# Kernel optimization log

Hardware: AMD Instinct MI355X
Metric: run time of the kernel (lower is better)

## Reference

```python
import jax, jax.numpy as jnp
import numpy as np

DIM, NHEADS, HEAD_DIM = 1536, 12, 128
EPS = 1e-6
ROPE_SPLIT = (22, 21, 21)  # head_dim//2 = 64 -> (c-2*(c//3), c//3, c//3)


def setup_inputs() -> dict:
    key = jax.random.key(0)
    ks = jax.random.split(key, 12)
    B, F, H, W = 1, 8, 16, 28
    L = F * H * W  # 3584
    inp = {
        "x": jax.random.normal(ks[0], (B, L, DIM), jnp.float32),
        "seq_lens": jnp.full((B,), L, dtype=jnp.int64),
        "grid_sizes": jnp.array([[F, H, W]] * B, dtype=jnp.int64),
        "freqs": jax.random.uniform(ks[1], (1024, HEAD_DIM // 2), jnp.float32) * (2 * np.pi),
        "Wq": jax.random.normal(ks[2], (DIM, DIM), jnp.float32) / np.sqrt(DIM),
        "bq": jnp.zeros((DIM,), jnp.float32),
        "Wk": jax.random.normal(ks[3], (DIM, DIM), jnp.float32) / np.sqrt(DIM),
        "bk": jnp.zeros((DIM,), jnp.float32),
        "Wv": jax.random.normal(ks[4], (DIM, DIM), jnp.float32) / np.sqrt(DIM),
        "bv": jnp.zeros((DIM,), jnp.float32),
        "Wo": jax.random.normal(ks[5], (DIM, DIM), jnp.float32) / np.sqrt(DIM),
        "bo": jnp.zeros((DIM,), jnp.float32),
        "gq": jnp.ones((DIM,), jnp.float32),
        "gk": jnp.ones((DIM,), jnp.float32),
    }
    return inp


def _rms_norm(x, g):
    var = jnp.mean(jnp.square(x), axis=-1, keepdims=True)
    return x * jax.lax.rsqrt(var + EPS) * g


def _rope_angles(freqs, F, H, W):
    # freqs: [1024, 64] angles; split per 3D axis and broadcast over the grid
    cf, ch, cw = ROPE_SPLIT
    af = freqs[:F, :cf]
    ah = freqs[:H, cf:cf + ch]
    aw = freqs[:W, cf + ch:]
    ang = jnp.concatenate([
        jnp.broadcast_to(af[:, None, None, :], (F, H, W, cf)),
        jnp.broadcast_to(ah[None, :, None, :], (F, H, W, ch)),
        jnp.broadcast_to(aw[None, None, :, :], (F, H, W, cw)),
    ], axis=-1).reshape(F * H * W, cf + ch + cw)  # [L, 64]
    return jnp.cos(ang), jnp.sin(ang)


def _rope_apply(x, cos, sin):
    # x: [B, L, N, D]; complex multiply by unit-modulus freqs, in real arithmetic
    b, s, n, d = x.shape
    xr = x.reshape(b, s, n, d // 2, 2)
    a, bi = xr[..., 0], xr[..., 1]
    c = cos[None, :, None, :]
    si = sin[None, :, None, :]
    out = jnp.stack([a * c - bi * si, a * si + bi * c], axis=-1)
    return out.reshape(b, s, n, d)


def reference(x, seq_lens, grid_sizes, freqs, Wq, bq, Wk, bk, Wv, bv, Wo, bo, gq, gk):
    b, s, _ = x.shape
    n, d = NHEADS, HEAD_DIM
    gs = np.asarray(grid_sizes)
    F, H, W = int(gs[0, 0]), int(gs[0, 1]), int(gs[0, 2])  # static grid (same per batch)

    q = _rms_norm(x @ Wq + bq, gq).reshape(b, s, n, d)
    k = _rms_norm(x @ Wk + bk, gk).reshape(b, s, n, d)
    v = (x @ Wv + bv).reshape(b, s, n, d)

    cos, sin = _rope_angles(freqs, F, H, W)
    q = _rope_apply(q, cos, sin)
    k = _rope_apply(k, cos, sin)

    # full attention with key-length masking (flash_attention k_lens semantics)
    scale = 1.0 / np.sqrt(d)
    scores = jnp.einsum("bqnd,bknd->bnqk", q, k) * scale
    key_mask = jnp.arange(s)[None, :] < seq_lens[:, None]  # [B, S]
    scores = jnp.where(key_mask[:, None, None, :], scores, -1e9)
    probs = jax.nn.softmax(scores, axis=-1)
    out = jnp.einsum("bnqk,bknd->bqnd", probs, v)

    return out.reshape(b, s, n * d) @ Wo + bo
```

## Files before the change

kernel.cpp:

```cpp
#include <hip/hip_runtime.h>

typedef __bf16 bf16;
typedef __bf16 bf16x8 __attribute__((ext_vector_type(8)));
typedef __bf16 bf16x4 __attribute__((ext_vector_type(4)));
typedef float f32x4 __attribute__((ext_vector_type(4)));

__device__ __forceinline__ void gload_lds16(const void* g, void* l) {
  __builtin_amdgcn_global_load_lds(
      (const __attribute__((address_space(1))) void*)g,
      (__attribute__((address_space(3))) void*)l, 16, 0, 0);
}

__device__ __forceinline__ bf16x8 ld8(const bf16* p) {
  bf16x8 v; __builtin_memcpy(&v, p, 16); return v;
}

__global__ __launch_bounds__(256) void prologue(
    const float* __restrict__ x, const float* __restrict__ Wq, const float* __restrict__ Wk,
    const float* __restrict__ Wv, const float* __restrict__ Wo,
    const float* __restrict__ freqs, const int* __restrict__ gs,
    const float* __restrict__ bq, const float* __restrict__ bk, const float* __restrict__ bv,
    bf16* __restrict__ x_bf, bf16* __restrict__ wqkvt, bf16* __restrict__ wot,
    float* __restrict__ tabc, float* __restrict__ tabs, float* __restrict__ bqkv) {
  __shared__ bf16 tile[64][72];
  int b = blockIdx.x, t = threadIdx.x;
  if (b < 2688) {
    int i = b * 256 + t;
    const float4* p = (const float4*)x + (size_t)i * 2;
    float4 a = p[0], v2 = p[1];
    bf16x8 o;
    o[0] = (bf16)a.x;  o[1] = (bf16)a.y;  o[2] = (bf16)a.z;  o[3] = (bf16)a.w;
    o[4] = (bf16)v2.x; o[5] = (bf16)v2.y; o[6] = (bf16)v2.z; o[7] = (bf16)v2.w;
    *((bf16x8*)x_bf + i) = o;
  } else if (b < 4992) {
    const float* W; bf16* dstM; int xy;
    if (b < 4416) {
      int idx = b - 2688; int z = idx / 576; xy = idx % 576;
      W = (z == 0) ? Wq : (z == 1) ? Wk : Wv;
      dstM = wqkvt + (size_t)z * 1536 * 1536;
    } else {
      xy = b - 4416; W = Wo; dstM = wot;
    }
    int k0 = (xy % 24) * 64, n0 = (xy / 24) * 64;
    int r = t >> 2, c0 = (t & 3) * 16;
    const float* src = W + (size_t)(k0 + r) * 1536 + n0 + c0;
#pragma unroll
    for (int q = 0; q < 4; ++q) {
      float4 v = *(const float4*)(src + q * 4);
      tile[c0 + q * 4 + 0][r] = (bf16)v.x;
      tile[c0 + q * 4 + 1][r] = (bf16)v.y;
      tile[c0 + q * 4 + 2][r] = (bf16)v.z;
      tile[c0 + q * 4 + 3][r] = (bf16)v.w;
    }
    __syncthreads();
    bf16* dst = dstM + (size_t)(n0 + r) * 1536 + k0 + c0;
    bf16x8 o0, o1;
#pragma unroll
    for (int j = 0; j < 8; ++j) { o0[j] = tile[r][c0 + j]; o1[j] = tile[r][c0 + 8 + j]; }
    *(bf16x8*)dst = o0;
    *(bf16x8*)(dst + 8) = o1;
  } else {
    int idx = (b - 4992) * 256 + t;
    if (idx < 4608)
      bqkv[idx] = (idx < 1536) ? bq[idx] : (idx < 3072) ? bk[idx - 1536] : bv[idx - 3072];
    int s = idx >> 6, i = idx & 63;
    int H = gs[1], Wd = gs[2];
    int f = s / (H * Wd);
    int rem = s - f * (H * Wd);
    int hh = rem / Wd;
    int ww = rem - hh * Wd;
    int row = (i < 22) ? f : ((i < 43) ? hh : ww);
    float a = freqs[row * 64 + i];
    tabc[idx] = cosf(a);
    tabs[idx] = sinf(a);
  }
}

template <typename OUT>
__global__ __launch_bounds__(256, 2) void gemm_bt(const bf16* __restrict__ A, const bf16* __restrict__ B,
                                                  const float* __restrict__ bias, OUT* __restrict__ C,
                                                  int M, int N, int K, int gx) {
  __shared__ bf16 As[128 * 32], Bs[128 * 32];
  int t = threadIdx.x, l = t & 63, w = t >> 6;
  int lane15 = l & 15, lhi = l >> 4;
  int b = blockIdx.x;
  int xcd = b & 7, idx = b >> 3;
  int g = xcd * ((int)gridDim.x >> 3) + idx;
  int m0 = (g % gx) * 128, n0 = (g / gx) * 128;
  int wm = (w >> 1) * 64, wn = (w & 1) * 64;
  f32x4 zero = {0.f, 0.f, 0.f, 0.f};
  f32x4 acc[4][4];
#pragma unroll
  for (int i = 0; i < 4; ++i)
#pragma unroll
    for (int j = 0; j < 4; ++j) acc[i][j] = zero;

  int srow = t >> 2, scol = (t & 3) * 8;
  const bf16* gA0 = A + (size_t)(m0 + srow) * K + scol;
  const bf16* gA1 = A + (size_t)(m0 + 64 + srow) * K + scol;
  const bf16* gB0 = B + (size_t)(n0 + srow) * K + scol;
  const bf16* gB1 = B + (size_t)(n0 + 64 + srow) * K + scol;
  char* ldsA = (char*)As + (size_t)w * 1024;
  char* ldsB = (char*)Bs + (size_t)w * 1024;

  for (int kt = 0; kt < K; kt += 32) {
    gload_lds16(gA0 + kt, ldsA);
    gload_lds16(gA1 + kt, ldsA + 4096);
    gload_lds16(gB0 + kt, ldsB);
    gload_lds16(gB1 + kt, ldsB + 4096);
    __syncthreads();
    bf16x8 af[4], bfr[4];
#pragma unroll
    for (int i = 0; i < 4; ++i) {
      af[i]  = ld8(&As[(wm + i * 16 + lane15) * 32 + lhi * 8]);
      bfr[i] = ld8(&Bs[(wn + i * 16 + lane15) * 32 + lhi * 8]);
    }
#pragma unroll
    for (int i = 0; i < 4; ++i)
#pragma unroll
      for (int j = 0; j < 4; ++j)
        acc[i][j] = __builtin_amdgcn_mfma_f32_16x16x32_bf16(af[i], bfr[j], acc[i][j], 0, 0, 0);
    __syncthreads();
  }
#pragma unroll
  for (int i = 0; i < 4; ++i)
#pragma unroll
    for (int j = 0; j < 4; ++j) {
      int col = n0 + wn + j * 16 + lane15;
      float bb = bias[col];
#pragma unroll
      for (int r = 0; r < 4; ++r) {
        int row = m0 + wm + i * 16 + lhi * 4 + r;
        C[(size_t)row * N + col] = (OUT)(acc[i][j][r] + bb);
      }
    }
}

__global__ __launch_bounds__(192) void postproc(const bf16* __restrict__ QKV,
    const float* __restrict__ gq, const float* __restrict__ gk,
    const float* __restrict__ tabc, const float* __restrict__ tabs,
    bf16* __restrict__ qb, bf16* __restrict__ kb) {
  int s = blockIdx.x, t = threadIdx.x;
  const bf16* Qr = QKV + (size_t)s * 4608;
  const bf16* Kr = Qr + 1536;
  int j0 = t * 8;
  bf16x8 qv8 = ld8(Qr + j0);
  bf16x8 kv8 = ld8(Kr + j0);
  float qv[8], kv[8];
  float sq = 0.f, sk = 0.f;
#pragma unroll
  for (int j = 0; j < 8; ++j) {
    qv[j] = (float)qv8[j]; sq += qv[j] * qv[j];
    kv[j] = (float)kv8[j]; sk += kv[j] * kv[j];
  }
#pragma unroll
  for (int off = 32; off > 0; off >>= 1) {
    sq += __shfl_down(sq, off);
    sk += __shfl_down(sk, off);
  }
  __shared__ float red[2][3];
  if ((t & 63) == 0) { red[0][t >> 6] = sq; red[1][t >> 6] = sk; }
  __syncthreads();
  float vq = red[0][0] + red[0][1] + red[0][2];
  float vk = red[1][0] + red[1][1] + red[1][2];
  float rq = 1.0f / sqrtf(vq * (1.0f / 1536.0f) + 1e-6f);
  float rk = 1.0f / sqrtf(vk * (1.0f / 1536.0f) + 1e-6f);
  rq *= 0.08838834764831845f;
  int i0 = (j0 >> 1) & 63;
  float4 cq = *(const float4*)(tabc + s * 64 + i0);
  float4 sq4 = *(const float4*)(tabs + s * 64 + i0);
  float cc[4] = {cq.x, cq.y, cq.z, cq.w};
  float sn[4] = {sq4.x, sq4.y, sq4.z, sq4.w};
  float4 g0 = *(const float4*)(gq + j0), g1 = *(const float4*)(gq + j0 + 4);
  float4 k0 = *(const float4*)(gk + j0), k1 = *(const float4*)(gk + j0 + 4);
  float gqa[8] = {g0.x, g0.y, g0.z, g0.w, g1.x, g1.y, g1.z, g1.w};
  float gka[8] = {k0.x, k0.y, k0.z, k0.w, k1.x, k1.y, k1.z, k1.w};
  int d0 = j0 & 127, h = j0 >> 7;
  bf16x8 qo, ko;
#pragma unroll
  for (int p = 0; p < 4; ++p) {
    float a = qv[2 * p] * rq * gqa[2 * p];
    float b = qv[2 * p + 1] * rq * gqa[2 * p + 1];
    qo[2 * p] = (bf16)(a * cc[p] - b * sn[p]);
    qo[2 * p + 1] = (bf16)(a * sn[p] + b * cc[p]);
    float ak = kv[2 * p] * rk * gka[2 * p];
    float bk2 = kv[2 * p + 1] * rk * gka[2 * p + 1];
    ko[2 * p] = (bf16)(ak * cc[p] - bk2 * sn[p]);
    ko[2 * p + 1] = (bf16)(ak * sn[p] + bk2 * cc[p]);
  }
  *(bf16x8*)(qb + (((size_t)h * 3584 + s) << 7) + d0) = qo;
  int sw = (s & 7) << 3;
  *(bf16x8*)(kb + (((size_t)(h * 56 + (s >> 6)) * 64 + (s & 63)) << 7) + (d0 ^ sw)) = ko;
}

__global__ __launch_bounds__(256) void transpose_v(const bf16* __restrict__ QKV,
                                                   bf16* __restrict__ vT) {
  __shared__ bf16 tile[128][72];
  int t = threadIdx.x;
  int h = blockIdx.y;
  int s0 = blockIdx.x * 64;
  int r = t >> 2, c0 = (t & 3) * 32;
  const bf16* src = QKV + (size_t)(s0 + r) * 4608 + 3072 + h * 128 + c0;
#pragma unroll
  for (int q = 0; q < 4; ++q) {
    bf16x8 v = ld8(src + q * 8);
#pragma unroll
    for (int j = 0; j < 8; ++j) tile[c0 + q * 8 + j][r] = v[j];
  }
  __syncthreads();
  int d = t >> 1, spHalf = t & 1;
  int sw = (d & 7) << 3;
  bf16* dstBase = vT + ((size_t)(h * 56 + blockIdx.x) * 128 + d) * 64;
#pragma unroll
  for (int q = 0; q < 4; ++q) {
    int mm = spHalf * 4 + q;
    int sA = 32 * (mm >> 2) + 16 * (mm & 1) + 4 * ((mm >> 1) & 1);
    bf16x4 lo, hi;
#pragma unroll
    for (int j = 0; j < 4; ++j) {
      lo[j] = tile[d][spHalf * 32 + q * 8 + j];
      hi[j] = tile[d][spHalf * 32 + q * 8 + 4 + j];
    }
    int slo = sA ^ sw;
    *(bf16x4*)(dstBase + slo) = lo;
    *(bf16x4*)(dstBase + (slo ^ 8)) = hi;
  }
}

__global__ __launch_bounds__(256, 2) void flash_attn(
    const bf16* __restrict__ qb, const bf16* __restrict__ kb, const bf16* __restrict__ vT,
    const int* __restrict__ sl, bf16* __restrict__ po0, bf16* __restrict__ po1,
    bf16* __restrict__ po2, bf16* __restrict__ po3, float* __restrict__ ml) {
  const int L = 3584;
  __shared__ bf16 Ks[64 * 128];
  __shared__ bf16 Vs[128 * 64];
  int t = threadIdx.x, l = t & 63, w = t >> 6;
  int lane15 = l & 15, lhi = l >> 4;
  int grp48 = l & 48;
  int b = blockIdx.x;
  int xcd = b & 7, k_ = b >> 3;
  int pg = k_ / 28, x = k_ - pg * 28;
  int p = pg * 8 + xcd;
  int h = p % 12, z = p / 12;
  int qw = x * 128 + w * 32;
  int seqlen = sl[0];
  bf16* po = (z == 0) ? po0 : (z == 1) ? po1 : (z == 2) ? po2 : po3;
  float* mlz = ml + (size_t)z * 12 * L * 2;

  bf16x8 aq[2][4];
#pragma unroll
  for (int qf = 0; qf < 2; ++qf)
#pragma unroll
    for (int kc = 0; kc < 4; ++kc)
      aq[qf][kc] = ld8(qb + (((size_t)h * L + qw + qf * 16 + lane15) << 7) + kc * 32 + lhi * 8);

  f32x4 zero = {0.f, 0.f, 0.f, 0.f};
  f32x4 out[2][8];
  float m2[2] = {-1e30f, -1e30f}, ls2[2] = {0.f, 0.f};
#pragma unroll
  for (int qf = 0; qf < 2; ++qf)
#pragma unroll
    for (int df = 0; df < 8; ++df) out[qf][df] = zero;

  int nt = (seqlen + 63) >> 6;
  if (nt > 56) nt = 56;
  int t0 = z * 14, t1 = t0 + 14;
  if (t0 > nt) t0 = nt;
  if (t1 > nt) t1 = nt;

  int src_off = w * 1024 + l * 16;
  char* ksd = (char*)Ks + w * 1024;
  char* vsd = (char*)Vs + w * 1024;

  for (int ti = t0; ti < t1; ++ti) {
    int kv0 = ti * 64;
    __syncthreads();
    {
      const char* kimg = (const char*)kb + ((size_t)(h * 56) + ti) * 16384;
      const char* vimg = (const char*)vT + ((size_t)(h * 56) + ti) * 16384;
#pragma unroll
      for (int pp = 0; pp < 4; ++pp) {
        gload_lds16(kimg + pp * 4096 + src_off, ksd + pp * 4096);
        gload_lds16(vimg + pp * 4096 + src_off, vsd + pp * 4096);
      }
    }
    __syncthreads();

    f32x4 sc[2][4];
#pragma unroll
    for (int qf = 0; qf < 2; ++qf)
#pragma unroll
      for (int a = 0; a < 4; ++a) sc[qf][a] = zero;
#pragma unroll
    for (int a = 0; a < 4; ++a) {
      int rk = a * 16 + lane15;
      const char* krow = (const char*)Ks + rk * 256;
      int swz = (rk & 7) << 4;
#pragma unroll
      for (int kc = 0; kc < 4; ++kc) {
        bf16x8 bk_ = ld8((const bf16*)(krow + ((kc * 64 + lhi * 16) ^ swz)));
        sc[0][a] = __builtin_amdgcn_mfma_f32_16x16x32_bf16(bk_, aq[0][kc], sc[0][a], 0, 0, 0);
        sc[1][a] = __builtin_amdgcn_mfma_f32_16x16x32_bf16(bk_, aq[1][kc], sc[1][a], 0, 0, 0);
      }
    }

    bool full = (kv0 + 64 <= seqlen);
    bf16x8 ap[2][2];
#pragma unroll
    for (int qf = 0; qf < 2; ++qf) {
      float tm = -1e30f;
#pragma unroll
      for (int a = 0; a < 4; ++a)
#pragma unroll
        for (int r = 0; r < 4; ++r) {
          float s = sc[qf][a][r];
          if (!full) {
            int col = kv0 + a * 16 + lhi * 4 + r;
            s = (col < seqlen) ? s : -1e30f;
            sc[qf][a][r] = s;
          }
          tm = fmaxf(tm, s);
        }
      tm = fmaxf(tm, __shfl_xor(tm, 16));
      tm = fmaxf(tm, __shfl_xor(tm, 32));
      if (!__all(tm <= m2[qf] + 8.0f)) {
        float nm = fmaxf(m2[qf], tm);
        float f = __expf(m2[qf] - nm);
        m2[qf] = nm;
        ls2[qf] *= f;
#pragma unroll
        for (int r = 0; r < 4; ++r) {
          float fr = __shfl(f, grp48 | (lhi * 4 + r));
#pragma unroll
          for (int df = 0; df < 8; ++df) out[qf][df][r] *= fr;
        }
      }
      float psum = 0.f;
#pragma unroll
      for (int a = 0; a < 4; ++a)
#pragma unroll
        for (int r = 0; r < 4; ++r) {
          float pv = __expf(sc[qf][a][r] - m2[qf]);
          sc[qf][a][r] = pv;
          psum += pv;
        }
      psum += __shfl_xor(psum, 16);
      psum += __shfl_xor(psum, 32);
      ls2[qf] += psum;
#pragma unroll
      for (int c = 0; c < 2; ++c) {
        bf16x8 f8;
#pragma unroll
        for (int r = 0; r < 4; ++r) {
          f8[r] = (bf16)sc[qf][2 * c][r];
          f8[r + 4] = (bf16)sc[qf][2 * c + 1][r];
        }
        ap[qf][c] = f8;
      }
    }

#pragma unroll
    for (int df = 0; df < 8; ++df) {
      int rd = df * 16 + lane15;
      const char* vrow2 = (const char*)Vs + rd * 128;
      int swz = (rd & 7) << 4;
#pragma unroll
      for (int c = 0; c < 2; ++c) {
        bf16x8 bv_ = ld8((const bf16*)(vrow2 + ((c * 64 + lhi * 16) ^ swz)));
        out[0][df] = __builtin_amdgcn_mfma_f32_16x16x32_bf16(ap[0][c], bv_, out[0][df], 0, 0, 0);
        out[1][df] = __builtin_amdgcn_mfma_f32_16x16x32_bf16(ap[1][c], bv_, out[1][df], 0, 0, 0);
      }
    }
  }

#pragma unroll
  for (int qf = 0; qf < 2; ++qf) {
#pragma unroll
    for (int r = 0; r < 4; ++r) {
      int row = qw + qf * 16 + lhi * 4 + r;
      size_t rbase = ((size_t)h * L + row) << 7;
#pragma unroll
      for (int df = 0; df < 8; ++df)
        po[rbase + df * 16 + lane15] = (bf16)out[qf][df][r];
    }
    if (lhi == 0) {
      int row = qw + qf * 16 + lane15;
      mlz[(((size_t)h * L + row) << 1)] = m2[qf];
      mlz[(((size_t)h * L + row) << 1) + 1] = ls2[qf];
    }
  }
}

__global__ __launch_bounds__(256) void combine4(
    const bf16* __restrict__ po0, const bf16* __restrict__ po1,
    const bf16* __restrict__ po2, const bf16* __restrict__ po3,
    const float* __restrict__ ml, bf16* __restrict__ attn) {
  const int L = 3584;
  int row = blockIdx.x * 16 + (threadIdx.x >> 4);
  int c0 = (threadIdx.x & 15) * 8;
  const size_t mls = (size_t)12 * L * 2;
  float m0 = ml[row * 2],           l0 = ml[row * 2 + 1];
  float m1 = ml[mls + row * 2],     l1 = ml[mls + row * 2 + 1];
  float m2 = ml[2 * mls + row * 2], l2 = ml[2 * mls + row * 2 + 1];
  float m3 = ml[3 * mls + row * 2], l3 = ml[3 * mls + row * 2 + 1];
  float M = fmaxf(fmaxf(m0, m1), fmaxf(m2, m3));
  float w0 = __expf(m0 - M), w1 = __expf(m1 - M);
  float w2 = __expf(m2 - M), w3 = __expf(m3 - M);
  float inv = 1.0f / fmaxf(w0 * l0 + w1 * l1 + w2 * l2 + w3 * l3, 1e-30f);
  bf16x8 a = ld8(po0 + (size_t)row * 128 + c0);
  bf16x8 b = ld8(po1 + (size_t)row * 128 + c0);
  bf16x8 c = ld8(po2 + (size_t)row * 128 + c0);
  bf16x8 d = ld8(po3 + (size_t)row * 128 + c0);
  int h = row / L, s = row % L;
  bf16x8 o;
#pragma unroll
  for (int j = 0; j < 8; ++j)
    o[j] = (bf16)((w0 * (float)a[j] + w1 * (float)b[j] + w2 * (float)c[j] + w3 * (float)d[j]) * inv);
  *(bf16x8*)(attn + (size_t)s * 1536 + h * 128 + c0) = o;
}

extern "C" void kernel_launch(void* const* d_in, const int* in_sizes, int n_in,
                              void* d_out, int out_size, void* d_ws, size_t ws_size,
                              hipStream_t stream) {
  const float* x = (const float*)d_in[0];
  const int* seq_lens = (const int*)d_in[1];
  const int* grid_sizes = (const int*)d_in[2];
  const float* freqs = (const float*)d_in[3];
  const float* Wq = (const float*)d_in[4];
  const float* bq = (const float*)d_in[5];
  const float* Wk = (const float*)d_in[6];
  const float* bk = (const float*)d_in[7];
  const float* Wv = (const float*)d_in[8];
  const float* bv = (const float*)d_in[9];
  const float* Wo = (const float*)d_in[10];
  const float* bo = (const float*)d_in[11];
  const float* gq = (const float*)d_in[12];
  const float* gk = (const float*)d_in[13];

  char* ws = (char*)d_ws;
  bf16* x_bf = (bf16*)(ws + 0);
  bf16* wqkvt = (bf16*)(ws + 11010048);
  bf16* wot = (bf16*)(ws + 25165824);
  float* bqkv = (float*)(ws + 29884416);
  bf16* QKV = (bf16*)(ws + 29902848);
  bf16* qb = (bf16*)(ws + 62932992);
  bf16* kb = (bf16*)(ws + 73943040);
  bf16* vT = (bf16*)(ws + 84953088);
  float* tabc = (float*)(ws + 95963136);
  float* tabs = (float*)(ws + 96880640);
  bf16* po0 = (bf16*)(ws + 29902848);
  bf16* attn = (bf16*)(ws + 51922944);
  bf16* po1 = (bf16*)(ws + 0);
  bf16* po2 = (bf16*)(ws + 11010048);
  float* ml  = (float*)(ws + 95963136);
  bf16* po3 = (bf16*)(ws + 97798144);

  prologue<<<5888, 256, 0, stream>>>(x, Wq, Wk, Wv, Wo, freqs, grid_sizes, bq, bk, bv,
                                     x_bf, wqkvt, wot, tabc, tabs, bqkv);
  gemm_bt<bf16><<<1008, 256, 0, stream>>>(x_bf, wqkvt, bqkv, QKV, 3584, 4608, 1536, 28);
  postproc<<<3584, 192, 0, stream>>>(QKV, gq, gk, tabc, tabs, qb, kb);
  transpose_v<<<dim3(56, 12), 256, 0, stream>>>(QKV, vT);
  flash_attn<<<1344, 256, 0, stream>>>(qb, kb, vT, seq_lens, po0, po1, po2, po3, ml);
  combine4<<<2688, 256, 0, stream>>>(po0, po1, po2, po3, ml, attn);
  gemm_bt<float><<<336, 256, 0, stream>>>(attn, wot, bo, (float*)d_out, 3584, 1536, 1536, 28);
}
```

Measured before the change: 261.2 us.

## Merge postproc with V transpose and use 64-row tiles for output GEMM

Combines the q/k norm+RoPE postprocessing and the V transpose into one launch by partitioning blocks, removing a kernel launch and letting both run concurrently. Replaces the output projection GEMM with a new 64x128 tile kernel launched with 672 blocks instead of 336, so more blocks are available across the CUs. The smaller tile lowers reuse per block and keeps single-buffered loads with two barriers per k-step. In the merged kernel, 64 of every 256 threads in the postproc blocks sit idle.

```diff
diff --git a/kernel.cpp b/kernel.cpp
--- a/kernel.cpp
+++ b/kernel.cpp
@@ -136,94 +136,144 @@
     }
 }
 
-__global__ __launch_bounds__(192) void postproc(const bf16* __restrict__ QKV,
+__global__ __launch_bounds__(256) void gemm_bt64(const bf16* __restrict__ A, const bf16* __restrict__ B,
+                                                 const float* __restrict__ bias, float* __restrict__ C,
+                                                 int M, int N, int K, int gx) {
+  __shared__ bf16 As[64 * 32], Bs[128 * 32];
+  int t = threadIdx.x, l = t & 63, w = t >> 6;
+  int lane15 = l & 15, lhi = l >> 4;
+  int b = blockIdx.x;
+  int xcd = b & 7, idx = b >> 3;
+  int g = xcd * ((int)gridDim.x >> 3) + idx;
+  int m0 = (g % gx) * 64, n0 = (g / gx) * 128;
+  int wm = w * 16;
+  f32x4 zero = {0.f, 0.f, 0.f, 0.f};
+  f32x4 acc[8];
+#pragma unroll
+  for (int j = 0; j < 8; ++j) acc[j] = zero;
+
+  int srow = t >> 2, scol = (t & 3) * 8;
+  const bf16* gA0 = A + (size_t)(m0 + srow) * K + scol;
+  const bf16* gB0 = B + (size_t)(n0 + srow) * K + scol;
+  const bf16* gB1 = B + (size_t)(n0 + 64 + srow) * K + scol;
+  char* ldsA = (char*)As + (size_t)w * 1024;
+  char* ldsB = (char*)Bs + (size_t)w * 1024;
+
+  for (int kt = 0; kt < K; kt += 32) {
+    gload_lds16(gA0 + kt, ldsA);
+    gload_lds16(gB0 + kt, ldsB);
+    gload_lds16(gB1 + kt, ldsB + 4096);
+    __syncthreads();
+    bf16x8 af = ld8(&As[(wm + lane15) * 32 + lhi * 8]);
+#pragma unroll
+    for (int j = 0; j < 8; ++j) {
+      bf16x8 bfr = ld8(&Bs[(j * 16 + lane15) * 32 + lhi * 8]);
+      acc[j] = __builtin_amdgcn_mfma_f32_16x16x32_bf16(af, bfr, acc[j], 0, 0, 0);
+    }
+    __syncthreads();
+  }
+#pragma unroll
+  for (int j = 0; j < 8; ++j) {
+    int col = n0 + j * 16 + lane15;
+    float bb = bias[col];
+#pragma unroll
+    for (int r = 0; r < 4; ++r) {
+      int row = m0 + wm + lhi * 4 + r;
+      C[(size_t)row * N + col] = acc[j][r] + bb;
+    }
+  }
+}
+
+__global__ __launch_bounds__(256) void postproc_v(const bf16* __restrict__ QKV,
     const float* __restrict__ gq, const float* __restrict__ gk,
     const float* __restrict__ tabc, const float* __restrict__ tabs,
-    bf16* __restrict__ qb, bf16* __restrict__ kb) {
-  int s = blockIdx.x, t = threadIdx.x;
-  const bf16* Qr = QKV + (size_t)s * 4608;
-  const bf16* Kr = Qr + 1536;
-  int j0 = t * 8;
-  bf16x8 qv8 = ld8(Qr + j0);
-  bf16x8 kv8 = ld8(Kr + j0);
-  float qv[8], kv[8];
-  float sq = 0.f, sk = 0.f;
-#pragma unroll
-  for (int j = 0; j < 8; ++j) {
-    qv[j] = (float)qv8[j]; sq += qv[j] * qv[j];
-    kv[j] = (float)kv8[j]; sk += kv[j] * kv[j];
-  }
-#pragma unroll
-  for (int off = 32; off > 0; off >>= 1) {
-    sq += __shfl_down(sq, off);
-    sk += __shfl_down(sk, off);
-  }
-  __shared__ float red[2][3];
-  if ((t & 63) == 0) { red[0][t >> 6] = sq; red[1][t >> 6] = sk; }
-  __syncthreads();
-  float vq = red[0][0] + red[0][1] + red[0][2];
-  float vk = red[1][0] + red[1][1] + red[1][2];
-  float rq = 1.0f / sqrtf(vq * (1.0f / 1536.0f) + 1e-6f);
-  float rk = 1.0f / sqrtf(vk * (1.0f / 1536.0f) + 1e-6f);
-  rq *= 0.08838834764831845f;
-  int i0 = (j0 >> 1) & 63;
-  float4 cq = *(const float4*)(tabc + s * 64 + i0);
-  float4 sq4 = *(const float4*)(tabs + s * 64 + i0);
-  float cc[4] = {cq.x, cq.y, cq.z, cq.w};
-  float sn[4] = {sq4.x, sq4.y, sq4.z, sq4.w};
-  float4 g0 = *(const float4*)(gq + j0), g1 = *(const float4*)(gq + j0 + 4);
-  float4 k0 = *(const float4*)(gk + j0), k1 = *(const float4*)(gk + j0 + 4);
-  float gqa[8] = {g0.x, g0.y, g0.z, g0.w, g1.x, g1.y, g1.z, g1.w};
-  float gka[8] = {k0.x, k0.y, k0.z, k0.w, k1.x, k1.y, k1.z, k1.w};
-  int d0 = j0 & 127, h = j0 >> 7;
-  bf16x8 qo, ko;
-#pragma unroll
-  for (int p = 0; p < 4; ++p) {
-    float a = qv[2 * p] * rq * gqa[2 * p];
-    float b = qv[2 * p + 1] * rq * gqa[2 * p + 1];
-    qo[2 * p] = (bf16)(a * cc[p] - b * sn[p]);
-    qo[2 * p + 1] = (bf16)(a * sn[p] + b * cc[p]);
-    float ak = kv[2 * p] * rk * gka[2 * p];
-    float bk2 = kv[2 * p + 1] * rk * gka[2 * p + 1];
-    ko[2 * p] = (bf16)(ak * cc[p] - bk2 * sn[p]);
-    ko[2 * p + 1] = (bf16)(ak * sn[p] + bk2 * cc[p]);
-  }
-  *(bf16x8*)(qb + (((size_t)h * 3584 + s) << 7) + d0) = qo;
-  int sw = (s & 7) << 3;
-  *(bf16x8*)(kb + (((size_t)(h * 56 + (s >> 6)) * 64 + (s & 63)) << 7) + (d0 ^ sw)) = ko;
-}
-
-__global__ __launch_bounds__(256) void transpose_v(const bf16* __restrict__ QKV,
-                                                   bf16* __restrict__ vT) {
+    bf16* __restrict__ qb, bf16* __restrict__ kb, bf16* __restrict__ vT) {
   __shared__ bf16 tile[128][72];
-  int t = threadIdx.x;
-  int h = blockIdx.y;
-  int s0 = blockIdx.x * 64;
-  int r = t >> 2, c0 = (t & 3) * 32;
-  const bf16* src = QKV + (size_t)(s0 + r) * 4608 + 3072 + h * 128 + c0;
-#pragma unroll
-  for (int q = 0; q < 4; ++q) {
-    bf16x8 v = ld8(src + q * 8);
-#pragma unroll
-    for (int j = 0; j < 8; ++j) tile[c0 + q * 8 + j][r] = v[j];
-  }
-  __syncthreads();
-  int d = t >> 1, spHalf = t & 1;
-  int sw = (d & 7) << 3;
-  bf16* dstBase = vT + ((size_t)(h * 56 + blockIdx.x) * 128 + d) * 64;
-#pragma unroll
-  for (int q = 0; q < 4; ++q) {
-    int mm = spHalf * 4 + q;
-    int sA = 32 * (mm >> 2) + 16 * (mm & 1) + 4 * ((mm >> 1) & 1);
-    bf16x4 lo, hi;
-#pragma unroll
-    for (int j = 0; j < 4; ++j) {
-      lo[j] = tile[d][spHalf * 32 + q * 8 + j];
-      hi[j] = tile[d][spHalf * 32 + q * 8 + 4 + j];
-    }
-    int slo = sA ^ sw;
-    *(bf16x4*)(dstBase + slo) = lo;
-    *(bf16x4*)(dstBase + (slo ^ 8)) = hi;
+  int b = blockIdx.x, t = threadIdx.x;
+  if (b < 3584) {
+    int s = b;
+    __shared__ float red[2][3];
+    float sq = 0.f, sk = 0.f;
+    float qv[8], kv[8];
+    int j0 = t * 8;
+    if (t < 192) {
+      const bf16* Qr = QKV + (size_t)s * 4608;
+      bf16x8 qv8 = ld8(Qr + j0);
+      bf16x8 kv8 = ld8(Qr + 1536 + j0);
+#pragma unroll
+      for (int j = 0; j < 8; ++j) {
+        qv[j] = (float)qv8[j]; sq += qv[j] * qv[j];
+        kv[j] = (float)kv8[j]; sk += kv[j] * kv[j];
+      }
+    }
+#pragma unroll
+    for (int off = 32; off > 0; off >>= 1) {
+      sq += __shfl_down(sq, off);
+      sk += __shfl_down(sk, off);
+    }
+    if ((t & 63) == 0 && t < 192) { red[0][t >> 6] = sq; red[1][t >> 6] = sk; }
+    __syncthreads();
+    if (t >= 192) return;
+    float vq = red[0][0] + red[0][1] + red[0][2];
+    float vk = red[1][0] + red[1][1] + red[1][2];
+    float rq = 1.0f / sqrtf(vq * (1.0f / 1536.0f) + 1e-6f);
+    float rk = 1.0f / sqrtf(vk * (1.0f / 1536.0f) + 1e-6f);
+    rq *= 0.08838834764831845f;
+    int i0 = (j0 >> 1) & 63;
+    float4 cq = *(const float4*)(tabc + s * 64 + i0);
+    float4 sq4 = *(const float4*)(tabs + s * 64 + i0);
+    float cc[4] = {cq.x, cq.y, cq.z, cq.w};
+    float sn[4] = {sq4.x, sq4.y, sq4.z, sq4.w};
+    float4 g0 = *(const float4*)(gq + j0), g1 = *(const float4*)(gq + j0 + 4);
+    float4 k0 = *(const float4*)(gk + j0), k1 = *(const float4*)(gk + j0 + 4);
+    float gqa[8] = {g0.x, g0.y, g0.z, g0.w, g1.x, g1.y, g1.z, g1.w};
+    float gka[8] = {k0.x, k0.y, k0.z, k0.w, k1.x, k1.y, k1.z, k1.w};
+    int d0 = j0 & 127, h = j0 >> 7;
+    bf16x8 qo, ko;
+#pragma unroll
+    for (int p = 0; p < 4; ++p) {
+      float a = qv[2 * p] * rq * gqa[2 * p];
+      float b2 = qv[2 * p + 1] * rq * gqa[2 * p + 1];
+      qo[2 * p] = (bf16)(a * cc[p] - b2 * sn[p]);
+      qo[2 * p + 1] = (bf16)(a * sn[p] + b2 * cc[p]);
+      float ak = kv[2 * p] * rk * gka[2 * p];
+      float bk2 = kv[2 * p + 1] * rk * gka[2 * p + 1];
+      ko[2 * p] = (bf16)(ak * cc[p] - bk2 * sn[p]);
+      ko[2 * p + 1] = (bf16)(ak * sn[p] + bk2 * cc[p]);
+    }
+    *(bf16x8*)(qb + (((size_t)h * 3584 + s) << 7) + d0) = qo;
+    int sw = (s & 7) << 3;
+    *(bf16x8*)(kb + (((size_t)(h * 56 + (s >> 6)) * 64 + (s & 63)) << 7) + (d0 ^ sw)) = ko;
+  } else {
+    int idx = b - 3584;
+    int xt = idx % 56, h = idx / 56;
+    int s0 = xt * 64;
+    int r = t >> 2, c0 = (t & 3) * 32;
+    const bf16* src = QKV + (size_t)(s0 + r) * 4608 + 3072 + h * 128 + c0;
+#pragma unroll
+    for (int q = 0; q < 4; ++q) {
+      bf16x8 v = ld8(src + q * 8);
+#pragma unroll
+      for (int j = 0; j < 8; ++j) tile[c0 + q * 8 + j][r] = v[j];
+    }
+    __syncthreads();
+    int d = t >> 1, spHalf = t & 1;
+    int sw = (d & 7) << 3;
+    bf16* dstBase = vT + ((size_t)(h * 56 + xt) * 128 + d) * 64;
+#pragma unroll
+    for (int q = 0; q < 4; ++q) {
+      int mm = spHalf * 4 + q;
+      int sA = 32 * (mm >> 2) + 16 * (mm & 1) + 4 * ((mm >> 1) & 1);
+      bf16x4 lo, hi;
+#pragma unroll
+      for (int j = 0; j < 4; ++j) {
+        lo[j] = tile[d][spHalf * 32 + q * 8 + j];
+        hi[j] = tile[d][spHalf * 32 + q * 8 + 4 + j];
+      }
+      int slo = sA ^ sw;
+      *(bf16x4*)(dstBase + slo) = lo;
+      *(bf16x4*)(dstBase + (slo ^ 8)) = hi;
+    }
   }
 }
 
@@ -458,9 +508,8 @@
   prologue<<<5888, 256, 0, stream>>>(x, Wq, Wk, Wv, Wo, freqs, grid_sizes, bq, bk, bv,
                                      x_bf, wqkvt, wot, tabc, tabs, bqkv);
   gemm_bt<bf16><<<1008, 256, 0, stream>>>(x_bf, wqkvt, bqkv, QKV, 3584, 4608, 1536, 28);
-  postproc<<<3584, 192, 0, stream>>>(QKV, gq, gk, tabc, tabs, qb, kb);
-  transpose_v<<<dim3(56, 12), 256, 0, stream>>>(QKV, vT);
+  postproc_v<<<4256, 256, 0, stream>>>(QKV, gq, gk, tabc, tabs, qb, kb, vT);
   flash_attn<<<1344, 256, 0, stream>>>(qb, kb, vT, seq_lens, po0, po1, po2, po3, ml);
   combine4<<<2688, 256, 0, stream>>>(po0, po1, po2, po3, ml, attn);
-  gemm_bt<float><<<336, 256, 0, stream>>>(attn, wot, bo, (float*)d_out, 3584, 1536, 1536, 28);
-}
+  gemm_bt64<<<672, 256, 0, stream>>>(attn, wot, bo, (float*)d_out, 3584, 1536, 1536, 56);
+}
```

After: 259.7 us. Within noise of the previous version (-0.6%).
